# Optimization experiments

Hardware: AMD Instinct MI355X
Metric: run time of the kernel (lower is better)

## Reference

```python
import jax, jax.numpy as jnp
import numpy as np

NUM_LAYERS = 4
INPUT_DIM = 512
BATCH = 16384


def setup_inputs() -> dict:
    key = jax.random.key(0)
    kx, kw, kb = jax.random.split(key, 3)
    x = jax.random.normal(kx, (BATCH, INPUT_DIM), dtype=jnp.float32)
    # PyTorch nn.Linear init: U(-1/sqrt(fan_in), 1/sqrt(fan_in))
    bound = 1.0 / np.sqrt(INPUT_DIM)
    W = jax.random.uniform(kw, (NUM_LAYERS, INPUT_DIM, INPUT_DIM), jnp.float32, -bound, bound)
    b = jax.random.uniform(kb, (NUM_LAYERS, INPUT_DIM), jnp.float32, -bound, bound)
    return {"x": x, "W": W, "b": b}


def reference(x, W, b):
    # x: [B, D]; W: [L, D, D] (torch Linear weight, so y = x @ W_i.T + b_i)
    x_list = [x]
    for i in range(NUM_LAYERS):
        x_ = x_list[-1]
        # sequentially accumulate dot-product residuals against all prior activations
        for x_pre in x_list[:-1]:
            s = jnp.sum(x_ * x_pre, axis=-1, keepdims=True)  # [B, 1]
            x_ = x_ + s
        y = jnp.einsum("bd,ed->be", x_, W[i]) + b[i]  # Linear: x_ @ W_i.T + b_i
        x_list.append(y)
    out = jnp.concatenate(x_list[1:], axis=-1)  # [B, L*D]
    return out
```

## Files before the change

kernel.cpp:

```cpp
#include <hip/hip_runtime.h>
#include <stdint.h>


#define BROWS 16384
#define DIM 512
#define NL 4
#define OUTSTRIDE (NL * DIM)

#define BM 64
#define BK 32
#define SEG (DIM / BK)
#define NSTEP (NL * SEG)

typedef unsigned short ushort_t;
typedef __attribute__((ext_vector_type(8))) short bf16x8;
typedef __attribute__((ext_vector_type(4))) float f32x4;

__device__ inline ushort_t f32_to_bf16(float f) {
    union { float f; uint32_t u; } v; v.f = f;
    uint32_t u = v.u;
    uint32_t r = (u + 0x7fffu + ((u >> 16) & 1u)) >> 16;
    return (ushort_t)r;
}

__device__ inline float bf16_bits_to_f32(ushort_t u) {
    union { uint32_t u; float f; } v; v.u = ((uint32_t)u) << 16; return v.f;
}

__device__ inline float bf16_lo(uint32_t p) {
    union { uint32_t u; float f; } v; v.u = p << 16; return v.f;
}
__device__ inline float bf16_hi(uint32_t p) {
    union { uint32_t u; float f; } v; v.u = p & 0xffff0000u; return v.f;
}

__device__ inline float wave_reduce_sum(float v) {
    #pragma unroll
    for (int off = 32; off > 0; off >>= 1) v += __shfl_down(v, off, 64);
    return v;
}

__global__ __launch_bounds__(256) void prep_kernel(
    const float* __restrict__ W, ushort_t* __restrict__ Wb,
    float* __restrict__ wsum)
{
    int row = blockIdx.x;
    int t = threadIdx.x;
    const float* wp = W + (size_t)row * DIM;
    float f0 = wp[2 * t], f1 = wp[2 * t + 1];
    ushort_t* wbp = Wb + (size_t)row * DIM;
    wbp[2 * t]     = f32_to_bf16(f0);
    wbp[2 * t + 1] = f32_to_bf16(f1);
    __shared__ float red[4];
    int wave = t >> 6, lane = t & 63;
    float r = wave_reduce_sum(f0 + f1);
    if (lane == 0) red[wave] = r;
    __syncthreads();
    if (t == 0) wsum[row] = red[0] + red[1] + red[2] + red[3];
}

__global__ __launch_bounds__(1024, 4) void cross_kernel(
    const float* __restrict__ x0,
    const ushort_t* __restrict__ Wb,
    const float* __restrict__ bias,
    const float* __restrict__ wsum,
    float* __restrict__ out)
{
    __shared__ __align__(16) ushort_t sAct[BM * DIM];
    __shared__ __align__(16) ushort_t sB[2][DIM * BK];
    __shared__ float sRed[4][8][BM];
    __shared__ float sSums[NL][BM];
    __shared__ float sCn[BM];

    const int tid  = threadIdx.x;
    const int wave = tid >> 6;
    const int lane = tid & 63;
    const int wm   = wave >> 3;
    const int wn8  = wave & 7;
    const int q    = lane >> 4;
    const int rr   = lane & 15;
    const int nlane = lane & 15;
    const int bm   = blockIdx.x * BM;

    const int srow = lane >> 2;

    auto stageB = [&](int s) {
        const ushort_t* gb = Wb + (size_t)(s >> 4) * (DIM * DIM) + (s & 15) * BK;
        #pragma unroll
        for (int c = 0; c < 2; ++c) {
            int r0 = wave * 32 + c * 16;
            int grow = r0 + srow;
            int gchunk = (lane & 3) ^ (grow & 3);
            __builtin_amdgcn_global_load_lds(
                (const __attribute__((address_space(1))) void*)(gb + (size_t)grow * DIM + gchunk * 8),
                (__attribute__((address_space(3))) void*)(&sB[s & 1][r0 * BK]), 16, 0, 0);
        }
    };

    stageB(0);

    #pragma unroll
    for (int r4 = 0; r4 < 4; ++r4) {
        int row = wave * 4 + r4;
        const float* xp = x0 + (size_t)(bm + row) * DIM + lane * 8;
        float4 a = ((const float4*)xp)[0];
        float4 b4 = ((const float4*)xp)[1];
        float f[8] = {a.x, a.y, a.z, a.w, b4.x, b4.y, b4.z, b4.w};
        bf16x8 o;
        float s = 0.f;
        #pragma unroll
        for (int i = 0; i < 8; ++i) { o[i] = (short)f32_to_bf16(f[i]); s += f[i]; }
        int kc = lane ^ (row & 15);
        *(bf16x8*)(&sAct[row * DIM + kc * 8]) = o;
        s = wave_reduce_sum(s);
        if (lane == 0) sSums[0][row] = s;
    }
    __syncthreads();

    uint32_t vk0[16], vk1[16];

    #pragma unroll
    for (int l = 0; l < NL; ++l) {
        f32x4 acc[2][4] = {};

        for (int t = 0; t < SEG; ++t) {
            int s = l * SEG + t;
            asm volatile("s_waitcnt vmcnt(0)" ::: "memory");
            __builtin_amdgcn_s_barrier();
            if (s + 1 < NSTEP) stageB(s + 1);

            bf16x8 af[2], bfr[4];
            #pragma unroll
            for (int mi = 0; mi < 2; ++mi) {
                int row = wm * 32 + mi * 16 + rr;
                int kc = (4 * t + q) ^ (row & 15);
                af[mi] = *(const bf16x8*)(&sAct[row * DIM + kc * 8]);
            }
            #pragma unroll
            for (int ni = 0; ni < 4; ++ni) {
                int erow = wn8 * 64 + ni * 16 + rr;
                int bc = q ^ (erow & 3);
                bfr[ni] = *(const bf16x8*)(&sB[s & 1][erow * BK + bc * 8]);
            }
            #pragma unroll
            for (int mi = 0; mi < 2; ++mi)
                #pragma unroll
                for (int ni = 0; ni < 4; ++ni)
                    acc[mi][ni] = __builtin_amdgcn_mfma_f32_16x16x32_bf16(
                        af[mi], bfr[ni], acc[mi][ni], 0, 0, 0);
        }

        __syncthreads();

        float ws4[4], bs4[4];
        #pragma unroll
        for (int ni = 0; ni < 4; ++ni) {
            int ng = wn8 * 64 + ni * 16 + nlane;
            ws4[ni] = wsum[l * DIM + ng];
            bs4[ni] = bias[l * DIM + ng];
        }

        #pragma unroll
        for (int mi = 0; mi < 2; ++mi)
            #pragma unroll
            for (int r = 0; r < 4; ++r) {
                const int mr = mi * 4 + r;
                const int row = wm * 32 + mi * 16 + q * 4 + r;
                float cc = (l == 0) ? 0.f : sCn[row];
                float vv[4];
                #pragma unroll
                for (int ni = 0; ni < 4; ++ni) {
                    vv[ni] = acc[mi][ni][r] + cc * ws4[ni] + bs4[ni];
                    int colg = wn8 * 64 + ni * 16 + nlane;
                    out[(size_t)(bm + row) * OUTSTRIDE + l * DIM + colg] = vv[ni];
                }
                if (l < 3) {
                    ushort_t xl[4];
                    #pragma unroll
                    for (int ni = 0; ni < 4; ++ni) {
                        int cg = wn8 * 8 + ni * 2 + (nlane >> 3);
                        int kc = cg ^ (row & 15);
                        xl[ni] = sAct[row * DIM + kc * 8 + (nlane & 7)];
                    }
                    float vs = 0.f, dc = 0.f;
                    #pragma unroll
                    for (int ni = 0; ni < 4; ++ni) {
                        vs += vv[ni];
                        dc += vv[ni] * bf16_bits_to_f32(xl[ni]);
                    }
                    float d0 = 0.f, d1 = 0.f, d2 = 0.f;
                    if (l == 0) {
                        d0 = dc;
                        #pragma unroll
                        for (int nip = 0; nip < 2; ++nip)
                            vk0[mr * 2 + nip] =
                                (uint32_t)xl[2 * nip] | ((uint32_t)xl[2 * nip + 1] << 16);
                    } else {
                        #pragma unroll
                        for (int nip = 0; nip < 2; ++nip) {
                            uint32_t p = vk0[mr * 2 + nip];
                            d0 += vv[2 * nip] * bf16_lo(p) + vv[2 * nip + 1] * bf16_hi(p);
                        }
                        if (l == 1) {
                            d1 = dc;
                            #pragma unroll
                            for (int nip = 0; nip < 2; ++nip)
                                vk1[mr * 2 + nip] =
                                    (uint32_t)xl[2 * nip] | ((uint32_t)xl[2 * nip + 1] << 16);
                        } else {
                            #pragma unroll
                            for (int nip = 0; nip < 2; ++nip) {
                                uint32_t p = vk1[mr * 2 + nip];
                                d1 += vv[2 * nip] * bf16_lo(p) + vv[2 * nip + 1] * bf16_hi(p);
                            }
                            d2 = dc;
                        }
                    }
                    #pragma unroll
                    for (int ni = 0; ni < 4; ++ni) {
                        int cg = wn8 * 8 + ni * 2 + (nlane >> 3);
                        int kc = cg ^ (row & 15);
                        sAct[row * DIM + kc * 8 + (nlane & 7)] = f32_to_bf16(vv[ni]);
                    }
                    #pragma unroll
                    for (int off = 8; off > 0; off >>= 1) {
                        vs += __shfl_xor(vs, off, 64);
                        d0 += __shfl_xor(d0, off, 64);
                        if (l >= 1) d1 += __shfl_xor(d1, off, 64);
                        if (l >= 2) d2 += __shfl_xor(d2, off, 64);
                    }
                    if (nlane == 0) {
                        sRed[0][wn8][row] = vs;
                        sRed[1][wn8][row] = d0;
                        if (l >= 1) sRed[2][wn8][row] = d1;
                        if (l >= 2) sRed[3][wn8][row] = d2;
                    }
                }
            }

        if (l < 3) {
            __syncthreads();
            if (tid < BM) {
                float vs = 0.f, d0 = 0.f;
                #pragma unroll
                for (int g = 0; g < 8; ++g) { vs += sRed[0][g][tid]; d0 += sRed[1][g][tid]; }
                float c = d0;
                if (l >= 1) {
                    float d1 = 0.f;
                    #pragma unroll
                    for (int g = 0; g < 8; ++g) d1 += sRed[2][g][tid];
                    c = c + d1 + c * sSums[1][tid];
                }
                if (l >= 2) {
                    float d2 = 0.f;
                    #pragma unroll
                    for (int g = 0; g < 8; ++g) d2 += sRed[3][g][tid];
                    c = c + d2 + c * sSums[2][tid];
                }
                sCn[tid] = c;
                sSums[l + 1][tid] = vs;
            }
            __syncthreads();
        }
    }
}

extern "C" void kernel_launch(void* const* d_in, const int* in_sizes, int n_in,
                              void* d_out, int out_size, void* d_ws, size_t ws_size,
                              hipStream_t stream) {
    (void)in_sizes; (void)n_in; (void)out_size; (void)ws_size;
    const float* x0   = (const float*)d_in[0];
    const float* W    = (const float*)d_in[1];
    const float* bias = (const float*)d_in[2];
    float* out = (float*)d_out;

    char* ws = (char*)d_ws;
    ushort_t* Wb   = (ushort_t*)ws;
    float*    wsum = (float*)(ws + 2097152);

    prep_kernel<<<NL * DIM, 256, 0, stream>>>(W, Wb, wsum);
    cross_kernel<<<BROWS / BM, 1024, 0, stream>>>(x0, Wb, bias, wsum, out);
}
```

Baseline: 264.8 us.

## Stage output tile through LDS for coalesced float4 stores, reuse B buffer

```diff
diff --git a/kernel.cpp b/kernel.cpp
--- a/kernel.cpp
+++ b/kernel.cpp
@@ -10,7 +10,6 @@
 #define BM 64
 #define BK 32
 #define SEG (DIM / BK)
-#define NSTEP (NL * SEG)
 
 typedef unsigned short ushort_t;
 typedef __attribute__((ext_vector_type(8))) short bf16x8;
@@ -59,7 +58,9 @@
     if (t == 0) wsum[row] = red[0] + red[1] + red[2] + red[3];
 }
 
-__global__ __launch_bounds__(1024, 4) void cross_kernel(
+__global__ __launch_bounds__(1024)
+__attribute__((amdgpu_waves_per_eu(4, 4)))
+void cross_kernel(
     const float* __restrict__ x0,
     const ushort_t* __restrict__ Wb,
     const float* __restrict__ bias,
@@ -67,10 +68,13 @@
     float* __restrict__ out)
 {
     __shared__ __align__(16) ushort_t sAct[BM * DIM];
-    __shared__ __align__(16) ushort_t sB[2][DIM * BK];
+    __shared__ __align__(16) unsigned char sBO[2 * DIM * BK * 2];
     __shared__ float sRed[4][8][BM];
     __shared__ float sSums[NL][BM];
     __shared__ float sCn[BM];
+
+    ushort_t* sB   = (ushort_t*)sBO;
+    float*    sOut = (float*)sBO;
 
     const int tid  = threadIdx.x;
     const int wave = tid >> 6;
@@ -93,7 +97,8 @@
             int gchunk = (lane & 3) ^ (grow & 3);
             __builtin_amdgcn_global_load_lds(
                 (const __attribute__((address_space(1))) void*)(gb + (size_t)grow * DIM + gchunk * 8),
-                (__attribute__((address_space(3))) void*)(&sB[s & 1][r0 * BK]), 16, 0, 0);
+                (__attribute__((address_space(3))) void*)(&sB[(size_t)(s & 1) * (DIM * BK) + r0 * BK]),
+                16, 0, 0);
         }
     };
 
@@ -127,7 +132,7 @@
             int s = l * SEG + t;
             asm volatile("s_waitcnt vmcnt(0)" ::: "memory");
             __builtin_amdgcn_s_barrier();
-            if (s + 1 < NSTEP) stageB(s + 1);
+            if (t + 1 < SEG) stageB(s + 1);
 
             bf16x8 af[2], bfr[4];
             #pragma unroll
@@ -140,7 +145,7 @@
             for (int ni = 0; ni < 4; ++ni) {
                 int erow = wn8 * 64 + ni * 16 + rr;
                 int bc = q ^ (erow & 3);
-                bfr[ni] = *(const bf16x8*)(&sB[s & 1][erow * BK + bc * 8]);
+                bfr[ni] = *(const bf16x8*)(&sB[(size_t)(t & 1) * (DIM * BK) + erow * BK + bc * 8]);
             }
             #pragma unroll
             for (int mi = 0; mi < 2; ++mi)
@@ -161,18 +166,18 @@
         }
 
         #pragma unroll
-        for (int mi = 0; mi < 2; ++mi)
+        for (int mi = 0; mi < 2; ++mi) {
             #pragma unroll
             for (int r = 0; r < 4; ++r) {
                 const int mr = mi * 4 + r;
                 const int row = wm * 32 + mi * 16 + q * 4 + r;
+                const int hrow = wm * 16 + q * 4 + r;
                 float cc = (l == 0) ? 0.f : sCn[row];
                 float vv[4];
                 #pragma unroll
                 for (int ni = 0; ni < 4; ++ni) {
                     vv[ni] = acc[mi][ni][r] + cc * ws4[ni] + bs4[ni];
-                    int colg = wn8 * 64 + ni * 16 + nlane;
-                    out[(size_t)(bm + row) * OUTSTRIDE + l * DIM + colg] = vv[ni];
+                    sOut[hrow * DIM + wn8 * 64 + ni * 16 + nlane] = vv[ni];
                 }
                 if (l < 3) {
                     ushort_t xl[4];
@@ -237,8 +242,21 @@
                     }
                 }
             }
-
-        if (l < 3) {
+            __syncthreads();
+            #pragma unroll
+            for (int it = 0; it < 4; ++it) {
+                int idx = it * 1024 + tid;
+                int hr = idx >> 7;
+                int c4 = idx & 127;
+                int grow = bm + (hr >> 4) * 32 + mi * 16 + (hr & 15);
+                float4 v4 = *(const float4*)&sOut[hr * DIM + c4 * 4];
+                *(float4*)&out[(size_t)grow * OUTSTRIDE + l * DIM + c4 * 4] = v4;
+            }
+            __syncthreads();
+        }
+
+        if (l < NL - 1) {
+            stageB((l + 1) * SEG);
             __syncthreads();
             if (tid < BM) {
                 float vs = 0.f, d0 = 0.f;
```

Measured after the change: 281.3 us. 1.06x slower.
